# Kernel optimization log

Measured on AMD Instinct MI355X. Metric: run time of the kernel, lower is better.

The kernel has to match this reference:

```python
import jax, jax.numpy as jnp
import numpy as np

S, XD, C, R = 6, 3, 8, 64   # num_freqs, x_dim, num_channels, res_scale
N = 262144
STD = 0.001


def setup_inputs() -> dict:
    key = jax.random.key(0)
    k1, k2, k3 = jax.random.split(key, 3)
    x = jax.random.uniform(k1, (N, XD), dtype=jnp.float32)
    features = jax.random.normal(k2, (S, 2 * XD, C, R, R), dtype=jnp.float32) * STD
    features_2d = jax.random.normal(k3, (S, 2 * XD, C, R, R), dtype=jnp.float32) * STD
    return {"x": x, "features": features, "features_2d": features_2d}


def _bilinear(img, gx, gy):
    # img: [C,H,W]; gx,gy: [P] normalized coords in [-1,1]
    # bilinear grid_sample, align_corners=True, clamped (border) indices
    _, H, W = img.shape
    ix = (gx + 1.0) * 0.5 * (W - 1)
    iy = (gy + 1.0) * 0.5 * (H - 1)
    ix0f = jnp.floor(ix)
    iy0f = jnp.floor(iy)
    wx = ix - ix0f
    wy = iy - iy0f
    ix0 = jnp.clip(ix0f.astype(jnp.int32), 0, W - 1)
    iy0 = jnp.clip(iy0f.astype(jnp.int32), 0, H - 1)
    ix1 = jnp.clip(ix0 + 1, 0, W - 1)
    iy1 = jnp.clip(iy0 + 1, 0, H - 1)
    v00 = img[:, iy0, ix0]  # [C,P]
    v01 = img[:, iy0, ix1]
    v10 = img[:, iy1, ix0]
    v11 = img[:, iy1, ix1]
    return (v00 * (1 - wx) * (1 - wy) + v01 * wx * (1 - wy)
            + v10 * (1 - wx) * wy + v11 * wx * wy)


def reference(x, features, features_2d):
    n = x.shape[0]
    scales = 2.0 ** jnp.arange(S, dtype=x.dtype)                   # [S]
    xb = x[:, None, :] * scales[:, None]                           # [N,S,3]
    latent = jnp.sin(jnp.stack([xb, xb + 0.5 * jnp.pi], axis=-2))  # [N,S,2,3]

    B = S * 2 * XD  # 36 independent (scale, sin/cos, dim) lookups

    # 1D (line) lookup: grid x-coord fixed at 0, y-coord = encoded value
    gy = jnp.transpose(latent.reshape(n, S, 2 * XD), (1, 2, 0)).reshape(B, n)
    gx = jnp.zeros_like(gy)
    fs = jax.vmap(_bilinear)(features.reshape(B, C, R, R), gx, gy)  # [B,C,N]
    fs = fs.reshape(S, 2, XD, C, n)

    # 2D (plane) lookup with cyclic dim pairs (1,2),(2,0),(0,1)
    pairs = jnp.array([[1, 2], [2, 0], [0, 1]])
    g2 = latent[..., pairs]                                        # [N,S,2,3,2]
    gx2 = jnp.transpose(g2[..., 0], (1, 2, 3, 0)).reshape(B, n)
    gy2 = jnp.transpose(g2[..., 1], (1, 2, 3, 0)).reshape(B, n)
    fs2 = jax.vmap(_bilinear)(features_2d.reshape(B, C, R, R), gx2, gy2)
    fs2 = fs2.reshape(S, 2, XD, C, n)

    out = jnp.transpose(fs * fs2, (4, 3, 0, 1, 2))                 # [N,C,S,2,3]
    out = out + latent[:, None]                                    # + PE, broadcast over C
    return out.reshape(n, C * S * 2 * XD)                          # [N, 288]
```

## Files before the change

kernel.cpp:

```cpp
#include <hip/hip_runtime.h>

#define NS 6
#define NXD 3
#define NC 8
#define NR 64
#define NB 36
#define NPOINTS 262144
#define OUTD 288
#define PTS 32

__device__ __forceinline__ unsigned short f2bf(float f) {
    unsigned u = __float_as_uint(f);
    unsigned r = u + 0x7fffu + ((u >> 16) & 1u);
    return (unsigned short)(r >> 16);
}
__device__ __forceinline__ unsigned pack2(float a, float b) {
    return (unsigned)f2bf(a) | ((unsigned)f2bf(b) << 16);
}

__global__ void build_px2(const float* __restrict__ F2, uint2* __restrict__ px) {
    int tid = blockIdx.x * 256 + threadIdx.x;
    const int total = NB * 64 * 64 * NC;
    if (tid >= total) return;
    int c  = tid & 7;
    int xx = (tid >> 3) & 63;
    int y  = (tid >> 9) & 63;
    int b  = tid >> 15;
    const float* img = F2 + (size_t)(b * NC + c) * (NR * NR);
    int x1 = xx < 63 ? xx + 1 : 63;
    int y1 = y  < 63 ? y  + 1 : 63;
    unsigned top = pack2(img[y  * NR + xx], img[y  * NR + x1]);
    unsigned bot = pack2(img[y1 * NR + xx], img[y1 * NR + x1]);
    px[tid] = make_uint2(top, bot);
}

__global__ void build_f1q(const float* __restrict__ F, unsigned* __restrict__ f1q) {
    int tid = blockIdx.x * 256 + threadIdx.x;
    const int total = NB * 64 * NC;
    if (tid >= total) return;
    int c = tid & 7;
    int y = (tid >> 3) & 63;
    int b = tid >> 9;
    const float* img = F + (size_t)(b * NC + c) * NR * NR;
    float a = 0.5f * (img[y * NR + 31] + img[y * NR + 32]);
    int y1 = y < 63 ? y + 1 : 63;
    float bb = 0.5f * (img[y1 * NR + 31] + img[y1 * NR + 32]);
    f1q[tid] = pack2(a, bb);
}

__global__ __launch_bounds__(256, 4) void encode_kernel(
    const float* __restrict__ x,
    const uint2* __restrict__ px,
    const unsigned* __restrict__ f1q,
    float* __restrict__ out)
{
    __shared__ float stage[PTS * 289];
    const int t = threadIdx.x;
    const int c = t & 7;
    const int u = t >> 3;
    const int n = blockIdx.x * PTS + u;

    const float xv0 = x[3 * n + 0];
    const float xv1 = x[3 * n + 1];
    const float xv2 = x[3 * n + 2];

    float* stg = &stage[u * 289];

    #pragma unroll
    for (int g = 0; g < 12; ++g) {
        const int s = g >> 1;
        const int p = g & 1;
        const float sc = (float)(1 << s);
        float l0, l1, l2;
        if (p == 0) {
            l0 = __sinf(xv0 * sc); l1 = __sinf(xv1 * sc); l2 = __sinf(xv2 * sc);
        } else {
            l0 = __cosf(xv0 * sc); l1 = __cosf(xv1 * sc); l2 = __cosf(xv2 * sc);
        }
        const int b0 = g * 3;
        #pragma unroll
        for (int k = 0; k < 3; ++k) {
            const int b = b0 + k;
            float gy1 = (k == 0) ? l0 : (k == 1) ? l1 : l2;
            float ga  = (k == 0) ? l1 : (k == 1) ? l2 : l0;
            float gb  = (k == 0) ? l2 : (k == 1) ? l0 : l1;

            float fy = fminf(fmaxf(__builtin_fmaf(gy1, 31.5f, 31.5f), 0.0f), 63.0f);
            float fy0 = floorf(fy);
            float wy = fy - fy0;
            int y0 = (int)fy0;
            unsigned pr = f1q[(b * 64 + y0) * 8 + c];
            float a0 = __uint_as_float(pr << 16);
            float a1 = __uint_as_float(pr & 0xffff0000u);
            float fsv = __builtin_fmaf(a1 - a0, wy, a0);

            float fx2 = fminf(fmaxf(__builtin_fmaf(ga, 31.5f, 31.5f), 0.0f), 63.0f);
            float fy2 = fminf(fmaxf(__builtin_fmaf(gb, 31.5f, 31.5f), 0.0f), 63.0f);
            float fx20 = floorf(fx2);
            float fy20 = floorf(fy2);
            float wx2 = fx2 - fx20;
            float wy2 = fy2 - fy20;
            int xx = (int)fx20;
            int yy = (int)fy20;
            uint2 pp = px[((b * 64 + yy) * 64 + xx) * 8 + c];
            float v00 = __uint_as_float(pp.x << 16);
            float v01 = __uint_as_float(pp.x & 0xffff0000u);
            float v10 = __uint_as_float(pp.y << 16);
            float v11 = __uint_as_float(pp.y & 0xffff0000u);
            float tp = __builtin_fmaf(v01 - v00, wx2, v00);
            float bt = __builtin_fmaf(v11 - v10, wx2, v10);
            float fs2v = __builtin_fmaf(bt - tp, wy2, tp);

            stg[c * 36 + b] = __builtin_fmaf(fsv, fs2v, gy1);
        }
    }
    __syncthreads();

    float* ob = out + (size_t)blockIdx.x * (PTS * OUTD);
    #pragma unroll
    for (int r = 0; r < 36; ++r) {
        int e = t + r * 256;
        int uu = e / 288;
        int v = e - uu * 288;
        ob[e] = stage[uu * 289 + v];
    }
}

extern "C" void kernel_launch(void* const* d_in, const int* in_sizes, int n_in,
                              void* d_out, int out_size, void* d_ws, size_t ws_size,
                              hipStream_t stream)
{
    const float* x  = (const float*)d_in[0];
    const float* F  = (const float*)d_in[1];
    const float* F2 = (const float*)d_in[2];
    float* out = (float*)d_out;

    uint2* px     = (uint2*)d_ws;
    unsigned* f1q = (unsigned*)((char*)d_ws + (size_t)NB * 64 * 64 * NC * 8);

    build_px2<<<(NB * 64 * 64 * NC + 255) / 256, 256, 0, stream>>>(F2, px);
    build_f1q<<<(NB * 64 * NC + 255) / 256, 256, 0, stream>>>(F, f1q);
    encode_kernel<<<NPOINTS / PTS, 256, 0, stream>>>(x, px, f1q, out);
}
```

Before: 381.3 us.

## Remap encode threads to one per (point, lookup) with vectorized 8-channel loads

Changes the work decomposition so each thread owns one of the 36 lookups for a point and loops over all 8 channels, instead of one thread per channel looping over 36 lookups. The 8 channel values for a lookup are contiguous, so each thread fetches them with wide uint4 loads (2 for the line table, 4 for the plane table) rather than 8 scattered narrow gathers. It also cuts redundant sin/cos and coordinate math, which was repeated across the 8 channel threads. Blocks grow to 576 threads with 16 points each, and the shared-memory write pattern changes to a stride of 36, which may cause bank conflicts.

```diff
diff --git a/kernel.cpp b/kernel.cpp
--- a/kernel.cpp
+++ b/kernel.cpp
@@ -7,7 +7,7 @@
 #define NB 36
 #define NPOINTS 262144
 #define OUTD 288
-#define PTS 32
+#define PTS 16
 
 __device__ __forceinline__ unsigned short f2bf(float f) {
     unsigned u = __float_as_uint(f);
@@ -48,7 +48,7 @@
     f1q[tid] = pack2(a, bb);
 }
 
-__global__ __launch_bounds__(256, 4) void encode_kernel(
+__global__ __launch_bounds__(576) void encode_kernel(
     const float* __restrict__ x,
     const uint2* __restrict__ px,
     const unsigned* __restrict__ f1q,
@@ -56,72 +56,77 @@
 {
     __shared__ float stage[PTS * 289];
     const int t = threadIdx.x;
-    const int c = t & 7;
-    const int u = t >> 3;
+    const int u = t / 36;
+    const int b = t - u * 36;
     const int n = blockIdx.x * PTS + u;
 
     const float xv0 = x[3 * n + 0];
     const float xv1 = x[3 * n + 1];
     const float xv2 = x[3 * n + 2];
 
-    float* stg = &stage[u * 289];
+    const int s  = b / 6;
+    const int rr = b - s * 6;
+    const int p  = rr / 3;
+    const int d  = rr - p * 3;
+    const float sc = (float)(1 << s);
 
+    float l0, l1, l2;
+    if (p == 0) { l0 = __sinf(xv0 * sc); l1 = __sinf(xv1 * sc); l2 = __sinf(xv2 * sc); }
+    else        { l0 = __cosf(xv0 * sc); l1 = __cosf(xv1 * sc); l2 = __cosf(xv2 * sc); }
+    const float gy1 = (d == 0) ? l0 : (d == 1) ? l1 : l2;
+    const float ga  = (d == 0) ? l1 : (d == 1) ? l2 : l0;
+    const float gb  = (d == 0) ? l2 : (d == 1) ? l0 : l1;
+
+    float fy  = fminf(fmaxf(__builtin_fmaf(gy1, 31.5f, 31.5f), 0.0f), 63.0f);
+    float fy0 = floorf(fy);
+    float wy  = fy - fy0;
+    int   y0  = (int)fy0;
+
+    float fx2  = fminf(fmaxf(__builtin_fmaf(ga, 31.5f, 31.5f), 0.0f), 63.0f);
+    float fy2  = fminf(fmaxf(__builtin_fmaf(gb, 31.5f, 31.5f), 0.0f), 63.0f);
+    float fx20 = floorf(fx2);
+    float fy20 = floorf(fy2);
+    float wx2  = fx2 - fx20;
+    float wy2  = fy2 - fy20;
+    int   xx   = (int)fx20;
+    int   yy   = (int)fy20;
+
+    const uint4* fp  = (const uint4*)(f1q + ((b * 64 + y0) * 8));
+    const uint4* pp4 = (const uint4*)(px + (((b * 64 + yy) * 64 + xx) * 8));
+    uint4 q0 = fp[0],  q1 = fp[1];
+    uint4 p0 = pp4[0], p1 = pp4[1], p2 = pp4[2], p3 = pp4[3];
+
+    const unsigned prs[8]  = {q0.x, q0.y, q0.z, q0.w, q1.x, q1.y, q1.z, q1.w};
+    const unsigned tops[8] = {p0.x, p0.z, p1.x, p1.z, p2.x, p2.z, p3.x, p3.z};
+    const unsigned bots[8] = {p0.y, p0.w, p1.y, p1.w, p2.y, p2.w, p3.y, p3.w};
+
+    float* stg = &stage[u * 289 + b];
     #pragma unroll
-    for (int g = 0; g < 12; ++g) {
-        const int s = g >> 1;
-        const int p = g & 1;
-        const float sc = (float)(1 << s);
-        float l0, l1, l2;
-        if (p == 0) {
-            l0 = __sinf(xv0 * sc); l1 = __sinf(xv1 * sc); l2 = __sinf(xv2 * sc);
-        } else {
-            l0 = __cosf(xv0 * sc); l1 = __cosf(xv1 * sc); l2 = __cosf(xv2 * sc);
-        }
-        const int b0 = g * 3;
-        #pragma unroll
-        for (int k = 0; k < 3; ++k) {
-            const int b = b0 + k;
-            float gy1 = (k == 0) ? l0 : (k == 1) ? l1 : l2;
-            float ga  = (k == 0) ? l1 : (k == 1) ? l2 : l0;
-            float gb  = (k == 0) ? l2 : (k == 1) ? l0 : l1;
+    for (int c = 0; c < 8; ++c) {
+        unsigned pr = prs[c];
+        float a0 = __uint_as_float(pr << 16);
+        float a1 = __uint_as_float(pr & 0xffff0000u);
+        float fsv = __builtin_fmaf(a1 - a0, wy, a0);
 
-            float fy = fminf(fmaxf(__builtin_fmaf(gy1, 31.5f, 31.5f), 0.0f), 63.0f);
-            float fy0 = floorf(fy);
-            float wy = fy - fy0;
-            int y0 = (int)fy0;
-            unsigned pr = f1q[(b * 64 + y0) * 8 + c];
-            float a0 = __uint_as_float(pr << 16);
-            float a1 = __uint_as_float(pr & 0xffff0000u);
-            float fsv = __builtin_fmaf(a1 - a0, wy, a0);
+        unsigned top = tops[c], bot = bots[c];
+        float v00 = __uint_as_float(top << 16);
+        float v01 = __uint_as_float(top & 0xffff0000u);
+        float v10 = __uint_as_float(bot << 16);
+        float v11 = __uint_as_float(bot & 0xffff0000u);
+        float tp  = __builtin_fmaf(v01 - v00, wx2, v00);
+        float bt  = __builtin_fmaf(v11 - v10, wx2, v10);
+        float fs2v = __builtin_fmaf(bt - tp, wy2, tp);
 
-            float fx2 = fminf(fmaxf(__builtin_fmaf(ga, 31.5f, 31.5f), 0.0f), 63.0f);
-            float fy2 = fminf(fmaxf(__builtin_fmaf(gb, 31.5f, 31.5f), 0.0f), 63.0f);
-            float fx20 = floorf(fx2);
-            float fy20 = floorf(fy2);
-            float wx2 = fx2 - fx20;
-            float wy2 = fy2 - fy20;
-            int xx = (int)fx20;
-            int yy = (int)fy20;
-            uint2 pp = px[((b * 64 + yy) * 64 + xx) * 8 + c];
-            float v00 = __uint_as_float(pp.x << 16);
-            float v01 = __uint_as_float(pp.x & 0xffff0000u);
-            float v10 = __uint_as_float(pp.y << 16);
-            float v11 = __uint_as_float(pp.y & 0xffff0000u);
-            float tp = __builtin_fmaf(v01 - v00, wx2, v00);
-            float bt = __builtin_fmaf(v11 - v10, wx2, v10);
-            float fs2v = __builtin_fmaf(bt - tp, wy2, tp);
-
-            stg[c * 36 + b] = __builtin_fmaf(fsv, fs2v, gy1);
-        }
+        stg[c * 36] = __builtin_fmaf(fsv, fs2v, gy1);
     }
     __syncthreads();
 
     float* ob = out + (size_t)blockIdx.x * (PTS * OUTD);
     #pragma unroll
-    for (int r = 0; r < 36; ++r) {
-        int e = t + r * 256;
+    for (int r = 0; r < 8; ++r) {
+        int e  = t + r * 576;
         int uu = e / 288;
-        int v = e - uu * 288;
+        int v  = e - uu * 288;
         ob[e] = stage[uu * 289 + v];
     }
 }
@@ -140,5 +145,5 @@
 
     build_px2<<<(NB * 64 * 64 * NC + 255) / 256, 256, 0, stream>>>(F2, px);
     build_f1q<<<(NB * 64 * NC + 255) / 256, 256, 0, stream>>>(F, f1q);
-    encode_kernel<<<NPOINTS / PTS, 256, 0, stream>>>(x, px, f1q, out);
+    encode_kernel<<<NPOINTS / PTS, 576, 0, stream>>>(x, px, f1q, out);
 }
```

Result: slower. 442.5 us (+16.1%).
